# Performance work log

Hardware: AMD Instinct MI355X
Metric: run time of the kernel (lower is better)

Reference implementation:

```python
import jax, jax.numpy as jnp
import numpy as np
import math

NB_STEPS = 50          # quadrature sub-intervals -> 51 Clenshaw-Curtis points
NUM_RNN_STEPS = 2


def _cc_weights(nb_steps):
    # Faithful port of UMNN's compute_cc_weights (Clenshaw-Curtis quadrature).
    lam = np.arange(0, nb_steps + 1).reshape(-1, 1).astype(np.float64)
    lam = np.cos((lam @ lam.T) * math.pi / nb_steps)
    lam[:, 0] = 0.5
    lam[:, -1] = 0.5 * lam[:, -1]
    lam = lam * 2.0 / nb_steps
    W = np.arange(0, nb_steps + 1).reshape(-1, 1).astype(np.float64)
    W[np.arange(1, nb_steps + 1, 2)] = 0
    W = 2.0 / (1.0 - W ** 2)
    W[0] = 1.0
    W[np.arange(1, nb_steps + 1, 2)] = 0
    cc = (lam.T @ W).astype(np.float32).reshape(-1)                      # [S]
    steps = np.cos(np.arange(0, nb_steps + 1) * math.pi / nb_steps).astype(np.float32)  # [S]
    return jnp.asarray(cc), jnp.asarray(steps)

CC_W, CC_STEPS = _cc_weights(NB_STEPS)  # S = NB_STEPS + 1 = 51


def _integrand(t, h, W1, b1, W2, b2, W3, b3, final_w):
    # IntegrandNN: MLP(cat(t,h)) -> ELU + 1 (>=0) -> fused power features -> ReLU(Linear)
    z = jnp.concatenate([t, h], axis=1)          # [N, in_d]
    z = jax.nn.relu(z @ W1.T + b1)               # [N, 128]
    z = jax.nn.relu(z @ W2.T + b2)               # [N, 128]
    z = jax.nn.elu(z @ W3.T + b3) + 1.0          # [N, 1], >= 0
    p = jnp.concatenate([z ** 1.5, z ** 2, z ** 2.5, z ** 3, z ** 3.5], axis=1)  # [N, 5]
    return jax.nn.relu((1.0 / (p + 1.0)) @ final_w.T)  # [N, 1]


def _inner_integral(x, h, params):
    # InnerUMNN: integral of IntegrandNN from x to xmax, xmax = max(x) + 10 (global scalar)
    N = x.shape[0]
    S = NB_STEPS + 1
    xmax = jnp.max(x) + 10.0
    T = x + (xmax - x) * (CC_STEPS[None, :] + 1.0) * 0.5   # [N, S]
    Tf = T.reshape(N * S, 1)
    hf = jnp.broadcast_to(h[:, None, :], (N, S, h.shape[1])).reshape(N * S, -1)
    g = _integrand(Tf, hf, *params).reshape(N, S)
    z = jnp.sum(g * CC_W[None, :], axis=1, keepdims=True)  # [N, 1]
    return z * (xmax - x) * 0.5


def _outer_integral(xT, h, params):
    # ParallelNeuralIntegral of InnerUMNN from x0 = 0 to xT; xT: [B, 1]
    B = xT.shape[0]
    S = NB_STEPS + 1
    X = xT * (CC_STEPS[None, :] + 1.0) * 0.5               # [B, S] (x0 = 0)
    Xf = X.reshape(B * S, 1)
    hf = jnp.broadcast_to(h[:, None, :], (B, S, h.shape[1])).reshape(B * S, -1)
    f = _inner_integral(Xf, hf, params).reshape(B, S)      # nested quadrature
    z = jnp.sum(f * CC_W[None, :], axis=1, keepdims=True)  # [B, 1]
    return z * xT * 0.5


def setup_inputs() -> dict:
    key = jax.random.key(0)
    ks = jax.random.split(key, 8)
    B, NF, IN_D, H = 256, 512, 64, 128
    x_ = jax.random.normal(ks[0], (B, NF), jnp.float32)
    h_ = jax.random.normal(ks[1], (B, IN_D - 1), jnp.float32)

    def lin(k, o, i):
        lim = 1.0 / np.sqrt(i)
        kw, kb = jax.random.split(k)
        return (jax.random.uniform(kw, (o, i), jnp.float32, -lim, lim),
                jax.random.uniform(kb, (o,), jnp.float32, -lim, lim))

    W1, b1 = lin(ks[2], H, IN_D)
    W2, b2 = lin(ks[3], H, H)
    W3, b3 = lin(ks[4], 1, H)
    lim5 = 1.0 / np.sqrt(5.0)
    final_w = jnp.abs(jax.random.uniform(ks[5], (1, 5), jnp.float32, -lim5, lim5))  # reset_params: abs
    log_weight = jnp.ones((1, NF), jnp.float32)            # reset_parameters: all ones
    sigmoid_param = jax.random.normal(ks[6], (1,), jnp.float32)
    return dict(x_=x_, h_=h_, W1=W1, b1=b1, W2=W2, b2=b2, W3=W3, b3=b3,
                final_w=final_w, log_weight=log_weight, sigmoid_param=sigmoid_param)


def reference(x_, h_, W1, b1, W2, b2, W3, b3, final_w, log_weight, sigmoid_param):
    params = (W1, b1, W2, b2, W3, b3, final_w)
    # compute_modular_function: F.linear then sum over dim 1 -> [B, 1]
    xm = jnp.sum(x_ @ log_weight.T, axis=1, keepdims=True)
    lam = jax.nn.sigmoid(sigmoid_param)                    # [1]
    out = jnp.zeros_like(xm)
    for _ in range(NUM_RNN_STEPS):
        xT = (1.0 - lam) * xm + lam * out
        out = _outer_integral(xT, h_, params)
    return out
```

## Files before the change

### kernel.cpp

```cpp
#include <hip/hip_runtime.h>
#include <math.h>

#define BB 256
#define NF 512
#define IND 64
#define HD 128
#define SS 51
#define NHM1 63

#define WS_LAM  0
#define WS_CCW  16
#define WS_U    80
#define WS_XM   144
#define WS_OUT1 656
#define WSH_C1  2048
#define WSH_W1  34816
#define WSH_W2F 40960
#define WS_W2F_F4 5120

typedef _Float16 f16x8 __attribute__((ext_vector_type(8)));
typedef float    f32x16 __attribute__((ext_vector_type(16)));

__global__ void k_setup(const float* __restrict__ x_, const float* __restrict__ h_,
                        const float* __restrict__ W1, const float* __restrict__ b1,
                        const float* __restrict__ W2, const float* __restrict__ lw,
                        const float* __restrict__ sp, float* __restrict__ ws) {
    int b = blockIdx.x;
    int j = threadIdx.x;
    short* wsh = (short*)ws;

    float acc = b1[j];
    const float* w1row = W1 + j * IND;
    const float* hrow  = h_ + b * NHM1;
    #pragma unroll 7
    for (int k = 0; k < NHM1; ++k) acc = fmaf(w1row[1 + k], hrow[k], acc);
    {
        _Float16 hv = (_Float16)acc;
        short sv; __builtin_memcpy(&sv, &hv, 2);
        wsh[WSH_C1 + b * HD + j] = sv;
    }

    float s = 0.f;
    for (int k = j; k < NF; k += HD) s = fmaf(x_[b * NF + k], lw[k], s);
    __shared__ float red[HD];
    red[j] = s;
    __syncthreads();
    for (int off = 64; off > 0; off >>= 1) {
        if (j < off) red[j] += red[j + off];
        __syncthreads();
    }
    if (j == 0) ws[WS_XM + b] = red[0];

    if (b < 128) {
        int d = b * 128 + j;
        int i = d & 7, lane = (d >> 3) & 63, kn = d >> 9;
        int kk = kn >> 2, nt = kn & 3;
        int row = nt * 32 + (lane & 31);
        int k = kk * 16 + (lane >> 5) * 8 + i;
        _Float16 hv = (_Float16)W2[row * HD + k];
        short sv; __builtin_memcpy(&sv, &hv, 2);
        wsh[WSH_W2F + d] = sv;
    }

    if (b == 0) {
        if (j < SS) {
            float acc2 = 0.f;
            for (int jj = 0; jj <= 50; jj += 2) {
                float wj = (jj == 0) ? 1.f : 2.f / (1.f - (float)(jj * jj));
                float lamv;
                if (j == 0 || j == 50) {
                    lamv = 0.02f;
                } else {
                    int m = (jj * j) % 100;
                    lamv = cosf((float)m * (float)M_PI / 50.f) * 0.04f;
                }
                acc2 = fmaf(lamv, wj, acc2);
            }
            ws[WS_CCW + j] = acc2;
            float st = cosf((float)j * (float)M_PI / 50.f);
            ws[WS_U + j] = (st + 1.f) * 0.5f;
        }
        if (j == 127) ws[WS_LAM] = 1.f / (1.f + expf(-sp[0]));
    }
    if (b == 2) {
        _Float16 hv = (_Float16)W1[j * IND];
        short sv; __builtin_memcpy(&sv, &hv, 2);
        wsh[WSH_W1 + j] = sv;
    }
    if (b == 4) ws[WS_OUT1 + j] = 0.f;
    if (b == 5) ws[WS_OUT1 + 128 + j] = 0.f;
}

__launch_bounds__(256, 2)
__global__ void k_int(const float* __restrict__ b2, const float* __restrict__ W3,
                      const float* __restrict__ b3, const float* __restrict__ fw,
                      const float* __restrict__ ws, const float* __restrict__ outprev,
                      float* __restrict__ tgt, float* __restrict__ ztgt) {
    int b = blockIdx.x >> 1, half = blockIdx.x & 1;
    int tid = threadIdx.x;
    int wv = tid >> 6, l = tid & 63;
    int c = l & 31, h = l >> 5;

    __shared__ __align__(16) short w2s[16384];
    __shared__ __align__(16) short c1s[HD];
    __shared__ __align__(16) short w1s[HD];
    __shared__ float us[SS], ccs[SS];
    __shared__ float wgt_s[4][64];
    __shared__ float xw[4];

    if (ztgt && half == 0 && tid == 0) ztgt[b] = 0.f;

    {
        const float4* src = reinterpret_cast<const float4*>(ws) + WS_W2F_F4;
        float4* dst = reinterpret_cast<float4*>(w2s);
        #pragma unroll
        for (int k = 0; k < 8; ++k) dst[tid + k * 256] = src[tid + k * 256];
    }
    if (tid < 16) {
        reinterpret_cast<float4*>(c1s)[tid] =
            reinterpret_cast<const float4*>((const short*)ws + WSH_C1 + b * HD)[tid];
    } else if (tid < 32) {
        reinterpret_cast<float4*>(w1s)[tid - 16] =
            reinterpret_cast<const float4*>((const short*)ws + WSH_W1)[tid - 16];
    }
    if (tid < SS) { us[tid] = ws[WS_U + tid]; ccs[tid] = ws[WS_CCW + tid]; }

    float lam = ws[WS_LAM];
    float xmv = ws[WS_XM + tid];
    float opv = outprev ? outprev[tid] : 0.f;
    float xtv = (1.f - lam) * xmv + lam * opv;
    float mx = fmaxf(xtv, 0.f);
    #pragma unroll
    for (int off = 32; off >= 1; off >>= 1) mx = fmaxf(mx, __shfl_xor(mx, off, 64));
    if (l == 0) xw[wv] = mx;
    __syncthreads();
    float xmax = fmaxf(fmaxf(xw[0], xw[1]), fmaxf(xw[2], xw[3])) + 10.f;
    float xT = (1.f - lam) * ws[WS_XM + b] + lam * (outprev ? outprev[b] : 0.f);

    const f16x8* w2v = reinterpret_cast<const f16x8*>(w2s);
    const f16x8* c1v = reinterpret_cast<const f16x8*>(c1s);
    const f16x8* w1v = reinterpret_cast<const f16x8*>(w1s);

    float b2n[4], w3n[4];
    #pragma unroll
    for (int nt = 0; nt < 4; ++nt) { b2n[nt] = b2[nt * 32 + c]; w3n[nt] = W3[nt * 32 + c]; }
    float b3v = b3[0];
    float fw0 = fw[0], fw1 = fw[1], fw2 = fw[2], fw3 = fw[3], fw4 = fw[4];

    float accO = 0.f;
    int start = half ? 21 : 0, end = half ? 41 : 21;

    for (int tl = start + wv; tl < end; tl += 4) {
        float t_[2];
        #pragma unroll
        for (int ti = 0; ti < 2; ++ti) {
            int m = tl * 64 + ti * 32 + c;
            int valid = (m <= 2600);
            int mm = valid ? m : 2600;
            int s  = (mm * 41121) >> 21;
            int si = mm - s * 51;
            float x = xT * us[s];
            float range = xmax - x;
            t_[ti] = fmaf(range, us[si], x);
            float wgt = valid ? (ccs[si] * ccs[s] * range * xT * 0.25f) : 0.f;
            if (h == 0) wgt_s[wv][ti * 32 + c] = wgt;
        }
        _Float16 th0 = (_Float16)t_[0], th1 = (_Float16)t_[1];
        f16x8 tv0 = {th0, th0, th0, th0, th0, th0, th0, th0};
        f16x8 tv1 = {th1, th1, th1, th1, th1, th1, th1, th1};
        f16x8 zf = {};

        f32x16 C[2][4];
        #pragma unroll
        for (int ti = 0; ti < 2; ++ti)
            #pragma unroll
            for (int nt = 0; nt < 4; ++nt)
                #pragma unroll
                for (int e = 0; e < 16; ++e) C[ti][nt][e] = 0.f;

        #pragma unroll
        for (int kk = 0; kk < 8; ++kk) {
            __builtin_amdgcn_sched_barrier(0);
            f16x8 c1p = c1v[kk * 2 + h];
            f16x8 w1p = w1v[kk * 2 + h];
            f16x8 A0 = __builtin_elementwise_max(__builtin_elementwise_fma(w1p, tv0, c1p), zf);
            f16x8 A1 = __builtin_elementwise_max(__builtin_elementwise_fma(w1p, tv1, c1p), zf);
            #pragma unroll
            for (int nt = 0; nt < 4; ++nt) {
                f16x8 Bf = w2v[(kk * 4 + nt) * 64 + l];
                C[0][nt] = __builtin_amdgcn_mfma_f32_32x32x16_f16(A0, Bf, C[0][nt], 0, 0, 0);
                C[1][nt] = __builtin_amdgcn_mfma_f32_32x32x16_f16(A1, Bf, C[1][nt], 0, 0, 0);
            }
        }
        __builtin_amdgcn_sched_barrier(0);

        #pragma unroll
        for (int ti = 0; ti < 2; ++ti) {
            float p[16];
            #pragma unroll
            for (int r = 0; r < 16; ++r) {
                float v = 0.f;
                #pragma unroll
                for (int nt = 0; nt < 4; ++nt) {
                    float a2 = fmaxf(C[ti][nt][r] + b2n[nt], 0.f);
                    v = fmaf(a2, w3n[nt], v);
                }
                p[r] = v;
            }
            float q8[8];
            { int bit = (l >> 4) & 1;
              #pragma unroll
              for (int r = 0; r < 8; ++r) {
                  float a = p[r], bb = p[r + 8];
                  float mine = bit ? bb : a, oth = bit ? a : bb;
                  q8[r] = mine + __shfl_xor(oth, 16, 64); } }
            float q4[4];
            { int bit = (l >> 3) & 1;
              #pragma unroll
              for (int r = 0; r < 4; ++r) {
                  float a = q8[r], bb = q8[r + 4];
                  float mine = bit ? bb : a, oth = bit ? a : bb;
                  q4[r] = mine + __shfl_xor(oth, 8, 64); } }
            float q2[2];
            { int bit = (l >> 2) & 1;
              #pragma unroll
              for (int r = 0; r < 2; ++r) {
                  float a = q4[r], bb = q4[r + 2];
                  float mine = bit ? bb : a, oth = bit ? a : bb;
                  q2[r] = mine + __shfl_xor(oth, 4, 64); } }
            float z1;
            { int bit = (l >> 1) & 1;
              float a = q2[0], bb = q2[1];
              float mine = bit ? bb : a, oth = bit ? a : bb;
              z1 = mine + __shfl_xor(oth, 2, 64); }
            z1 += __shfl_xor(z1, 1, 64);

            if (!(l & 1)) {
                int r = (l >> 1) & 15;
                int m_local = (r & 3) + 8 * (r >> 2) + 4 * h;
                float zs = z1 + b3v;
                float z = zs > 0.f ? zs + 1.f : __expf(zs);
                float sq = sqrtf(z);
                float p15 = z * sq, p2 = z * z, p25 = p2 * sq, p3 = p2 * z, p35 = p3 * sq;
                float g = fw0 * __builtin_amdgcn_rcpf(p15 + 1.f)
                        + fw1 * __builtin_amdgcn_rcpf(p2  + 1.f)
                        + fw2 * __builtin_amdgcn_rcpf(p25 + 1.f)
                        + fw3 * __builtin_amdgcn_rcpf(p3  + 1.f)
                        + fw4 * __builtin_amdgcn_rcpf(p35 + 1.f);
                g = fmaxf(g, 0.f);
                accO = fmaf(g, wgt_s[wv][ti * 32 + m_local], accO);
            }
        }
    }

    #pragma unroll
    for (int off = 32; off >= 1; off >>= 1) accO += __shfl_xor(accO, off, 64);
    if (l == 0) atomicAdd(&tgt[b], accO);
}

extern "C" void kernel_launch(void* const* d_in, const int* in_sizes, int n_in,
                              void* d_out, int out_size, void* d_ws, size_t ws_size,
                              hipStream_t stream) {
    (void)in_sizes; (void)n_in; (void)out_size; (void)ws_size;
    const float* x_ = (const float*)d_in[0];
    const float* h_ = (const float*)d_in[1];
    const float* W1 = (const float*)d_in[2];
    const float* b1 = (const float*)d_in[3];
    const float* W2 = (const float*)d_in[4];
    const float* b2 = (const float*)d_in[5];
    const float* W3 = (const float*)d_in[6];
    const float* b3 = (const float*)d_in[7];
    const float* fw = (const float*)d_in[8];
    const float* lw = (const float*)d_in[9];
    const float* sp = (const float*)d_in[10];
    float* wsf  = (float*)d_ws;
    float* out1 = wsf + WS_OUT1;
    float* out  = (float*)d_out;

    k_setup<<<BB, HD, 0, stream>>>(x_, h_, W1, b1, W2, lw, sp, wsf);
    k_int<<<BB * 2, 256, 0, stream>>>(b2, W3, b3, fw, wsf, nullptr, out1, out);
    k_int<<<BB * 2, 256, 0, stream>>>(b2, W3, b3, fw, wsf, out1, out, nullptr);
}
```

Before: 79.10 us.

## Keep W2 fragments in registers and split hidden dim across waves

Each wave now owns a 32-column slice of the second layer and holds its W2 fragments, c1 and w1 in registers loaded straight from the workspace, in place of staging all of W2 in LDS. All four waves process the same 64 points per iteration and exchange partial dot products through a double-buffered shared array with a block barrier each iteration; wave 0 applies the final nonlinearity and accumulates the quadrature. This removes the 32KB LDS staging and most LDS reads of B fragments, and it shrinks accumulator count. In exchange it adds a __syncthreads per iteration, and three of the four waves sit idle during the epilogue.

```diff
diff --git a/kernel.cpp b/kernel.cpp
--- a/kernel.cpp
+++ b/kernel.cpp
@@ -16,7 +16,6 @@
 #define WSH_C1  2048
 #define WSH_W1  34816
 #define WSH_W2F 40960
-#define WS_W2F_F4 5120
 
 typedef _Float16 f16x8 __attribute__((ext_vector_type(8)));
 typedef float    f32x16 __attribute__((ext_vector_type(16)));
@@ -99,30 +98,12 @@
     int b = blockIdx.x >> 1, half = blockIdx.x & 1;
     int tid = threadIdx.x;
     int wv = tid >> 6, l = tid & 63;
-    int c = l & 31, h = l >> 5;
-
-    __shared__ __align__(16) short w2s[16384];
-    __shared__ __align__(16) short c1s[HD];
-    __shared__ __align__(16) short w1s[HD];
-    __shared__ float us[SS], ccs[SS];
-    __shared__ float wgt_s[4][64];
-    __shared__ float xw[4];
+    int e32 = l & 31, h2 = l >> 5;
+
+    __shared__ float us[SS], ccs[SS], xw[4];
+    __shared__ float part[2][2][4][32];
 
     if (ztgt && half == 0 && tid == 0) ztgt[b] = 0.f;
-
-    {
-        const float4* src = reinterpret_cast<const float4*>(ws) + WS_W2F_F4;
-        float4* dst = reinterpret_cast<float4*>(w2s);
-        #pragma unroll
-        for (int k = 0; k < 8; ++k) dst[tid + k * 256] = src[tid + k * 256];
-    }
-    if (tid < 16) {
-        reinterpret_cast<float4*>(c1s)[tid] =
-            reinterpret_cast<const float4*>((const short*)ws + WSH_C1 + b * HD)[tid];
-    } else if (tid < 32) {
-        reinterpret_cast<float4*>(w1s)[tid - 16] =
-            reinterpret_cast<const float4*>((const short*)ws + WSH_W1)[tid - 16];
-    }
     if (tid < SS) { us[tid] = ws[WS_U + tid]; ccs[tid] = ws[WS_CCW + tid]; }
 
     float lam = ws[WS_LAM];
@@ -137,125 +118,101 @@
     float xmax = fmaxf(fmaxf(xw[0], xw[1]), fmaxf(xw[2], xw[3])) + 10.f;
     float xT = (1.f - lam) * ws[WS_XM + b] + lam * (outprev ? outprev[b] : 0.f);
 
-    const f16x8* w2v = reinterpret_cast<const f16x8*>(w2s);
-    const f16x8* c1v = reinterpret_cast<const f16x8*>(c1s);
-    const f16x8* w1v = reinterpret_cast<const f16x8*>(w1s);
-
-    float b2n[4], w3n[4];
+    const short* wsh = (const short*)ws;
+
+    f16x8 Af[8], c1r[8], w1r[8];
     #pragma unroll
-    for (int nt = 0; nt < 4; ++nt) { b2n[nt] = b2[nt * 32 + c]; w3n[nt] = W3[nt * 32 + c]; }
+    for (int kk = 0; kk < 8; ++kk) {
+        Af[kk]  = *reinterpret_cast<const f16x8*>(wsh + WSH_W2F + ((kk * 4 + wv) * 64 + l) * 8);
+        c1r[kk] = *reinterpret_cast<const f16x8*>(wsh + WSH_C1 + b * HD + kk * 16 + h2 * 8);
+        w1r[kk] = *reinterpret_cast<const f16x8*>(wsh + WSH_W1 + kk * 16 + h2 * 8);
+    }
+    float b2n[16], w3n[16];
+    #pragma unroll
+    for (int r = 0; r < 16; ++r) {
+        int j = wv * 32 + (r & 3) + 8 * (r >> 2) + 4 * h2;
+        b2n[r] = b2[j]; w3n[r] = W3[j];
+    }
     float b3v = b3[0];
     float fw0 = fw[0], fw1 = fw[1], fw2 = fw[2], fw3 = fw[3], fw4 = fw[4];
 
     float accO = 0.f;
-    int start = half ? 21 : 0, end = half ? 41 : 21;
-
-    for (int tl = start + wv; tl < end; tl += 4) {
+    int buf = 0;
+    int base0 = half * 1344;
+
+    for (int it = 0; it < 21; ++it) {
+        int base = base0 + it * 64;
         float t_[2];
         #pragma unroll
         for (int ti = 0; ti < 2; ++ti) {
-            int m = tl * 64 + ti * 32 + c;
+            int m = base + ti * 32 + e32;
+            int mm = m <= 2600 ? m : 2600;
+            int s  = (mm * 41121) >> 21;
+            int si = mm - s * 51;
+            float x = xT * us[s];
+            t_[ti] = fmaf(xmax - x, us[si], x);
+        }
+        _Float16 th0 = (_Float16)t_[0], th1 = (_Float16)t_[1];
+        f16x8 tv0 = {th0, th0, th0, th0, th0, th0, th0, th0};
+        f16x8 tv1 = {th1, th1, th1, th1, th1, th1, th1, th1};
+        f16x8 zf = {};
+
+        f32x16 C0, C1;
+        #pragma unroll
+        for (int e = 0; e < 16; ++e) { C0[e] = 0.f; C1[e] = 0.f; }
+
+        #pragma unroll
+        for (int kk = 0; kk < 8; ++kk) {
+            f16x8 B0 = __builtin_elementwise_max(__builtin_elementwise_fma(w1r[kk], tv0, c1r[kk]), zf);
+            f16x8 B1 = __builtin_elementwise_max(__builtin_elementwise_fma(w1r[kk], tv1, c1r[kk]), zf);
+            C0 = __builtin_amdgcn_mfma_f32_32x32x16_f16(Af[kk], B0, C0, 0, 0, 0);
+            C1 = __builtin_amdgcn_mfma_f32_32x32x16_f16(Af[kk], B1, C1, 0, 0, 0);
+            __builtin_amdgcn_sched_barrier(0);
+        }
+
+        {
+            float s0 = 0.f;
+            #pragma unroll
+            for (int r = 0; r < 16; ++r) s0 = fmaf(fmaxf(C0[r] + b2n[r], 0.f), w3n[r], s0);
+            s0 += __shfl_xor(s0, 32, 64);
+            if (h2 == 0) part[buf][0][wv][e32] = s0;
+            float s1 = 0.f;
+            #pragma unroll
+            for (int r = 0; r < 16; ++r) s1 = fmaf(fmaxf(C1[r] + b2n[r], 0.f), w3n[r], s1);
+            s1 += __shfl_xor(s1, 32, 64);
+            if (h2 == 0) part[buf][1][wv][e32] = s1;
+        }
+        __syncthreads();
+
+        if (wv == 0) {
+            int m = base + l;
+            float zs = part[buf][h2][0][e32] + part[buf][h2][1][e32]
+                     + part[buf][h2][2][e32] + part[buf][h2][3][e32] + b3v;
+            float z = zs > 0.f ? zs + 1.f : __expf(zs);
+            float sq = sqrtf(z);
+            float p15 = z * sq, p2 = z * z, p25 = p2 * sq, p3 = p2 * z, p35 = p3 * sq;
+            float g = fw0 * __builtin_amdgcn_rcpf(p15 + 1.f)
+                    + fw1 * __builtin_amdgcn_rcpf(p2  + 1.f)
+                    + fw2 * __builtin_amdgcn_rcpf(p25 + 1.f)
+                    + fw3 * __builtin_amdgcn_rcpf(p3  + 1.f)
+                    + fw4 * __builtin_amdgcn_rcpf(p35 + 1.f);
+            g = fmaxf(g, 0.f);
             int valid = (m <= 2600);
             int mm = valid ? m : 2600;
             int s  = (mm * 41121) >> 21;
             int si = mm - s * 51;
             float x = xT * us[s];
-            float range = xmax - x;
-            t_[ti] = fmaf(range, us[si], x);
-            float wgt = valid ? (ccs[si] * ccs[s] * range * xT * 0.25f) : 0.f;
-            if (h == 0) wgt_s[wv][ti * 32 + c] = wgt;
-        }
-        _Float16 th0 = (_Float16)t_[0], th1 = (_Float16)t_[1];
-        f16x8 tv0 = {th0, th0, th0, th0, th0, th0, th0, th0};
-        f16x8 tv1 = {th1, th1, th1, th1, th1, th1, th1, th1};
-        f16x8 zf = {};
-
-        f32x16 C[2][4];
-        #pragma unroll
-        for (int ti = 0; ti < 2; ++ti)
-            #pragma unroll
-            for (int nt = 0; nt < 4; ++nt)
-                #pragma unroll
-                for (int e = 0; e < 16; ++e) C[ti][nt][e] = 0.f;
-
-        #pragma unroll
-        for (int kk = 0; kk < 8; ++kk) {
-            __builtin_amdgcn_sched_barrier(0);
-            f16x8 c1p = c1v[kk * 2 + h];
-            f16x8 w1p = w1v[kk * 2 + h];
-            f16x8 A0 = __builtin_elementwise_max(__builtin_elementwise_fma(w1p, tv0, c1p), zf);
-            f16x8 A1 = __builtin_elementwise_max(__builtin_elementwise_fma(w1p, tv1, c1p), zf);
-            #pragma unroll
-            for (int nt = 0; nt < 4; ++nt) {
-                f16x8 Bf = w2v[(kk * 4 + nt) * 64 + l];
-                C[0][nt] = __builtin_amdgcn_mfma_f32_32x32x16_f16(A0, Bf, C[0][nt], 0, 0, 0);
-                C[1][nt] = __builtin_amdgcn_mfma_f32_32x32x16_f16(A1, Bf, C[1][nt], 0, 0, 0);
-            }
-        }
-        __builtin_amdgcn_sched_barrier(0);
-
-        #pragma unroll
-        for (int ti = 0; ti < 2; ++ti) {
-            float p[16];
-            #pragma unroll
-            for (int r = 0; r < 16; ++r) {
-                float v = 0.f;
-                #pragma unroll
-                for (int nt = 0; nt < 4; ++nt) {
-                    float a2 = fmaxf(C[ti][nt][r] + b2n[nt], 0.f);
-                    v = fmaf(a2, w3n[nt], v);
-                }
-                p[r] = v;
-            }
-            float q8[8];
-            { int bit = (l >> 4) & 1;
-              #pragma unroll
-              for (int r = 0; r < 8; ++r) {
-                  float a = p[r], bb = p[r + 8];
-                  float mine = bit ? bb : a, oth = bit ? a : bb;
-                  q8[r] = mine + __shfl_xor(oth, 16, 64); } }
-            float q4[4];
-            { int bit = (l >> 3) & 1;
-              #pragma unroll
-              for (int r = 0; r < 4; ++r) {
-                  float a = q8[r], bb = q8[r + 4];
-                  float mine = bit ? bb : a, oth = bit ? a : bb;
-                  q4[r] = mine + __shfl_xor(oth, 8, 64); } }
-            float q2[2];
-            { int bit = (l >> 2) & 1;
-              #pragma unroll
-              for (int r = 0; r < 2; ++r) {
-                  float a = q4[r], bb = q4[r + 2];
-                  float mine = bit ? bb : a, oth = bit ? a : bb;
-                  q2[r] = mine + __shfl_xor(oth, 4, 64); } }
-            float z1;
-            { int bit = (l >> 1) & 1;
-              float a = q2[0], bb = q2[1];
-              float mine = bit ? bb : a, oth = bit ? a : bb;
-              z1 = mine + __shfl_xor(oth, 2, 64); }
-            z1 += __shfl_xor(z1, 1, 64);
-
-            if (!(l & 1)) {
-                int r = (l >> 1) & 15;
-                int m_local = (r & 3) + 8 * (r >> 2) + 4 * h;
-                float zs = z1 + b3v;
-                float z = zs > 0.f ? zs + 1.f : __expf(zs);
-                float sq = sqrtf(z);
-                float p15 = z * sq, p2 = z * z, p25 = p2 * sq, p3 = p2 * z, p35 = p3 * sq;
-                float g = fw0 * __builtin_amdgcn_rcpf(p15 + 1.f)
-                        + fw1 * __builtin_amdgcn_rcpf(p2  + 1.f)
-                        + fw2 * __builtin_amdgcn_rcpf(p25 + 1.f)
-                        + fw3 * __builtin_amdgcn_rcpf(p3  + 1.f)
-                        + fw4 * __builtin_amdgcn_rcpf(p35 + 1.f);
-                g = fmaxf(g, 0.f);
-                accO = fmaf(g, wgt_s[wv][ti * 32 + m_local], accO);
-            }
-        }
-    }
-
-    #pragma unroll
-    for (int off = 32; off >= 1; off >>= 1) accO += __shfl_xor(accO, off, 64);
-    if (l == 0) atomicAdd(&tgt[b], accO);
+            float wgt = valid ? (ccs[si] * ccs[s] * (xmax - x) * xT * 0.25f) : 0.f;
+            accO = fmaf(g, wgt, accO);
+        }
+        buf ^= 1;
+    }
+
+    if (wv == 0) {
+        #pragma unroll
+        for (int off = 32; off >= 1; off >>= 1) accO += __shfl_xor(accO, off, 64);
+        if (l == 0) atomicAdd(&tgt[b], accO);
+    }
 }
 
 extern "C" void kernel_launch(void* const* d_in, const int* in_sizes, int n_in,
```

Measured after the change: 78.55 us. About the same (-0.7%).
